# Performance work log

Measured on AMD Instinct MI355X. Metric: run time of the kernel, lower is better.

## Reference

```python
import jax, jax.numpy as jnp
import numpy as np

CODEBOOK_SIZE = 1024
EMBEDDING_DIM = 256
COMMITMENT_COST = 0.25


def setup_inputs() -> dict:
    key = jax.random.key(0)
    k1, k2 = jax.random.split(key)
    x = jax.random.normal(k1, (32, EMBEDDING_DIM, 32, 32), dtype=jnp.float32)
    # embedding initialized uniform(-1/K, 1/K) like the torch module
    embedding = jax.random.uniform(
        k2, (CODEBOOK_SIZE, EMBEDDING_DIM), dtype=jnp.float32,
        minval=-1.0 / CODEBOOK_SIZE, maxval=1.0 / CODEBOOK_SIZE)
    return {"x": x, "embedding": embedding}


def reference(x, embedding):
    # x: [B, C, H, W] -> inputs: [B, H, W, C]
    inputs = jnp.transpose(x, (0, 2, 3, 1))
    input_shape = inputs.shape
    flat = inputs.reshape(-1, EMBEDDING_DIM)  # [N, D]
    # squared L2 distances to codebook: [N, K]
    distances = (jnp.sum(flat ** 2, axis=1, keepdims=True)
                 + jnp.sum(embedding ** 2, axis=1)
                 - 2.0 * flat @ embedding.T)
    encoding_indices = jnp.argmin(distances, axis=1)  # [N]
    encodings = jax.nn.one_hot(encoding_indices, CODEBOOK_SIZE, dtype=jnp.float32)  # [N, K]
    # gather (same math as encodings @ embedding)
    quantized = embedding[encoding_indices].reshape(input_shape)  # [B, H, W, C]
    e_latent_loss = jnp.mean((jax.lax.stop_gradient(quantized) - inputs) ** 2)
    q_latent_loss = jnp.mean((quantized - jax.lax.stop_gradient(inputs)) ** 2)
    loss = q_latent_loss + COMMITMENT_COST * e_latent_loss
    # straight-through estimator
    quantized_st = inputs + jax.lax.stop_gradient(quantized - inputs)
    return (loss, jnp.transpose(quantized_st, (0, 3, 1, 2)), encodings)
```

## Files before the change

### kernel.cpp

```cpp
#include <hip/hip_runtime.h>
#include <cstdint>
#include <cstddef>

constexpr int B = 32, C = 256, H = 32, W = 32;
constexpr int NPTS = B * H * W;
constexpr int DIM  = 256;
constexpr int K    = 1024;
constexpr int QELEMS = B * C * H * W;
constexpr int CHW = C * H * W;

typedef __attribute__((ext_vector_type(8))) short s8v;
typedef __attribute__((ext_vector_type(4))) float f32x4;

#define GLD_LDS16(g, l)                                                        \
  __builtin_amdgcn_global_load_lds(                                            \
      (const __attribute__((address_space(1))) unsigned int*)(g),              \
      (__attribute__((address_space(3))) unsigned int*)(l), 16, 0, 0)

__device__ __forceinline__ unsigned short f2bf(float f) {
  unsigned u = __float_as_uint(f);
  return (unsigned short)((u + 0x7FFFu + ((u >> 16) & 1u)) >> 16);
}

__global__ __launch_bounds__(256) void prep_kernel(
    const float* __restrict__ x, const float* __restrict__ emb,
    unsigned short* __restrict__ ehi, float* __restrict__ esq,
    unsigned short* __restrict__ xhi, float* __restrict__ xsq,
    float* __restrict__ encz) {
  __shared__ float xls[DIM][32];
  const int t = threadIdx.x;
  const int bid = blockIdx.x;

  if (bid < 16) {
    float (*sums)[64] = (float (*)[64])xls;
    const int k = bid * 64 + (t & 63);
    const int seg = t >> 6;
    const float* er = emb + (size_t)k * DIM + seg * 64;
    float v[64];
    float4* v4 = (float4*)v;
#pragma unroll
    for (int i = 0; i < 16; ++i) v4[i] = *(const float4*)(er + i * 4);
    float s = 0.f;
#pragma unroll
    for (int i = 0; i < 64; ++i) s = fmaf(v[i], v[i], s);
    unsigned short* eo = ehi + (size_t)k * DIM + seg * 64;
#pragma unroll
    for (int i = 0; i < 8; ++i) {
      unsigned short h[8];
#pragma unroll
      for (int j = 0; j < 8; ++j) h[j] = f2bf(v[i * 8 + j]);
      *(s8v*)(eo + i * 8) = *(s8v*)h;
    }
    sums[seg][t & 63] = s;
    __syncthreads();
    if (t < 64)
      esq[bid * 64 + t] =
          ((sums[0][t] + sums[1][t]) + sums[2][t]) + sums[3][t];
    return;
  }

  const int u = bid - 16;
  const int g = u / 3, r = u - g * 3;

  if (r != 0) {
    const size_t bidx = (size_t)g * 2 + (r - 1);
    float* sl = encz + bidx * 16384;
    float4* b4 = (float4*)(sl + 3);
    const float4 z4 = {0.f, 0.f, 0.f, 0.f};
#pragma unroll
    for (int j = 0; j < 16; ++j) {
      const int idx = t + j * 256;
      if (idx < 4095) b4[idx] = z4;
    }
    if (t == 0) { sl[0] = 0.f; sl[1] = 0.f; sl[2] = 0.f; sl[16383] = 0.f; }
    return;
  }

  const int n0 = g * 32;
  const int bb = n0 >> 10, hw0 = n0 & 1023;
  const float* xb = x + (size_t)bb * CHW + hw0;
  const int lane = t & 63, w = t >> 6;
  const int row_off = lane >> 3;
  const int p4 = (lane & 7) * 4;
#pragma unroll
  for (int i = 0; i < 8; ++i) {
    const int c0 = w * 64 + i * 8;
    GLD_LDS16(xb + (size_t)(c0 + row_off) * 1024 + p4, &xls[c0][0]);
  }
  __syncthreads();

  if (t < 32) {
    float s = 0.f;
#pragma unroll 8
    for (int c = 0; c < 256; ++c) {
      const float v = xls[c][t];
      s = fmaf(v, v, s);
    }
    xsq[n0 + t] = s;
  }
  const int p2 = t & 31, cb = (t >> 5) * 32;
  unsigned short* xo = xhi + (size_t)(n0 + p2) * DIM + cb;
#pragma unroll
  for (int i = 0; i < 4; ++i) {
    unsigned short h[8];
#pragma unroll
    for (int j = 0; j < 8; ++j) h[j] = f2bf(xls[cb + i * 8 + j][p2]);
    *(s8v*)(xo + i * 8) = *(s8v*)h;
  }
}

constexpr float MARGIN = 1e-3f;
__global__ __launch_bounds__(256) void coarse_kernel(
    const unsigned short* __restrict__ xhi, const unsigned short* __restrict__ ehi,
    const float* __restrict__ esq, const float* __restrict__ xsq,
    float* __restrict__ part, unsigned int* __restrict__ cand) {
  __shared__ __align__(16) unsigned short xs[128][32];
  __shared__ __align__(16) unsigned short es[128][32];
  __shared__ float xsq_s[128], esq_s[128], thr_s[128];
  __shared__ unsigned long long red2[2][128];
  __shared__ unsigned int cntL[128];

  const int t = threadIdx.x;
  const int lane = t & 63, w = t >> 6;
  const int wn = (w & 1) * 64, wk = (w >> 1) * 64;
  const int col = lane & 15, quad = lane >> 4;
  const int nblk = blockIdx.x * 128;
  const int kblk = blockIdx.y * 128;

  if (t < 128) {
    xsq_s[t] = xsq[nblk + t];
    esq_s[t] = esq[kblk + t];
    cntL[t] = 0u;
  }

  f32x4 acc[4][4];
#pragma unroll
  for (int i = 0; i < 4; ++i)
#pragma unroll
    for (int j = 0; j < 4; ++j) acc[i][j] = (f32x4){0.f, 0.f, 0.f, 0.f};

  const int gl_row = lane >> 2;
  const int gl_c   = (lane & 3) * 8;

  for (int c0 = 0; c0 < DIM; c0 += 32) {
    __syncthreads();
#pragma unroll
    for (int i = 0; i < 2; ++i) {
      const int inst = w + 4 * i;
      const int row = inst * 16 + gl_row;
      GLD_LDS16(xhi + (size_t)(nblk + row) * DIM + c0 + gl_c, &xs[inst * 16][0]);
      GLD_LDS16(ehi + (size_t)(kblk + row) * DIM + c0 + gl_c, &es[inst * 16][0]);
    }
    __syncthreads();
    s8v a[4], b[4];
#pragma unroll
    for (int ti = 0; ti < 4; ++ti)
      a[ti] = *(const s8v*)&xs[wn + ti * 16 + col][quad * 8];
#pragma unroll
    for (int tj = 0; tj < 4; ++tj)
      b[tj] = *(const s8v*)&es[wk + tj * 16 + col][quad * 8];
#pragma unroll
    for (int ti = 0; ti < 4; ++ti)
#pragma unroll
      for (int tj = 0; tj < 4; ++tj)
        acc[ti][tj] = __builtin_amdgcn_mfma_f32_16x16x32_bf16(
            a[ti], b[tj], acc[ti][tj], 0, 0, 0);
  }

  unsigned long long nmin[4][4];
#pragma unroll
  for (int ti = 0; ti < 4; ++ti)
#pragma unroll
    for (int r = 0; r < 4; ++r) nmin[ti][r] = ~0ULL;
#pragma unroll
  for (int ti = 0; ti < 4; ++ti)
#pragma unroll
    for (int tj = 0; tj < 4; ++tj) {
      const int krel = wk + tj * 16 + col;
      const float eq = esq_s[krel];
#pragma unroll
      for (int r = 0; r < 4; ++r) {
        const int nl = wn + ti * 16 + quad * 4 + r;
        const float d = (xsq_s[nl] + eq) - 2.f * acc[ti][tj][r];
        const unsigned long long key =
            ((unsigned long long)__float_as_uint(d) << 32) |
            (unsigned)(kblk + krel);
        if (key < nmin[ti][r]) nmin[ti][r] = key;
      }
    }
#pragma unroll
  for (int o = 1; o < 16; o <<= 1)
#pragma unroll
    for (int ti = 0; ti < 4; ++ti)
#pragma unroll
      for (int r = 0; r < 4; ++r) {
        const unsigned long long v = __shfl_xor(nmin[ti][r], o, 64);
        if (v < nmin[ti][r]) nmin[ti][r] = v;
      }
  if (col == 0) {
#pragma unroll
    for (int ti = 0; ti < 4; ++ti)
#pragma unroll
      for (int r = 0; r < 4; ++r)
        red2[w >> 1][wn + ti * 16 + quad * 4 + r] = nmin[ti][r];
  }
  __syncthreads();
  if (t < 128) {
    const unsigned long long m0 = red2[0][t], m1 = red2[1][t];
    const unsigned long long m = (m1 < m0) ? m1 : m0;
    const float dmin = __uint_as_float((unsigned)(m >> 32));
    part[(size_t)(nblk + t) * 8 + blockIdx.y] = dmin;
    thr_s[t] = dmin + MARGIN;
  }
  __syncthreads();
#pragma unroll
  for (int ti = 0; ti < 4; ++ti)
#pragma unroll
    for (int tj = 0; tj < 4; ++tj) {
      const int krel = wk + tj * 16 + col;
      const float eq = esq_s[krel];
#pragma unroll
      for (int r = 0; r < 4; ++r) {
        const int nl = wn + ti * 16 + quad * 4 + r;
        const float d = (xsq_s[nl] + eq) - 2.f * acc[ti][tj][r];
        if (d <= thr_s[nl]) {
          const unsigned slot = atomicAdd(&cntL[nl], 1u);
          if (slot < 4u)
            cand[((size_t)(nblk + nl) * 8 + blockIdx.y) * 4 + slot] =
                (unsigned)(kblk + krel);
        }
      }
    }
  __syncthreads();
  if (t < 128) {
    unsigned c = cntL[t];
    const size_t base = ((size_t)(nblk + t) * 8 + blockIdx.y) * 4;
    if (c > 4u) { cand[base + 3] = 0xFFFFFFFEu; c = 3u; }
    for (unsigned s = c; s < 4u; ++s) cand[base + s] = 0xFFFFFFFFu;
  }
}

__global__ __launch_bounds__(256) void finish_kernel(
    const float* __restrict__ x, const float* __restrict__ emb,
    const float* __restrict__ esq, const float* __restrict__ xsq,
    const float* __restrict__ part, const unsigned int* __restrict__ cand,
    float* __restrict__ outq, float* __restrict__ enc,
    float* __restrict__ lws) {
  __shared__ __align__(16) float xls[DIM][17];
  __shared__ unsigned list[512];
  __shared__ unsigned long long best[16];
  __shared__ float thr_s[16];
  __shared__ float xsq_s[16];
  __shared__ float lred[4];
  __shared__ int ids[16];
  __shared__ int lcnt;

  const int t = threadIdx.x;
  const int n0 = blockIdx.x * 16;
  const int bb = n0 >> 10, hw0 = n0 & 1023;

  const float* xb = x + (size_t)bb * CHW + hw0;
  {
    const int p = t & 15, cs = t >> 4;
#pragma unroll 4
    for (int r = 0; r < 16; ++r) {
      const int c = r * 16 + cs;
      xls[c][p] = xb[(size_t)c * 1024 + p];
    }
  }
  if (t == 0) lcnt = 0;
  if (t < 16) {
    best[t] = ~0ULL;
    xsq_s[t] = xsq[n0 + t];
    const float4 p0 = *(const float4*)&part[(size_t)(n0 + t) * 8];
    const float4 p1 = *(const float4*)&part[(size_t)(n0 + t) * 8 + 4];
    float g = fminf(fminf(fminf(p0.x, p0.y), fminf(p0.z, p0.w)),
                    fminf(fminf(p1.x, p1.y), fminf(p1.z, p1.w)));
    thr_s[t] = g + MARGIN;
  }
  __syncthreads();

  if (t < 128) {
    const int nn = t >> 3, s = t & 7;
    const float pv = part[(size_t)(n0 + nn) * 8 + s];
    if (pv <= thr_s[nn]) {
      const uint4 c4 = *(const uint4*)&cand[((size_t)(n0 + nn) * 8 + s) * 4];
      const unsigned vs[4] = {c4.x, c4.y, c4.z, c4.w};
#pragma unroll
      for (int i = 0; i < 4; ++i) {
        const unsigned v = vs[i];
        if (v == 0xFFFFFFFFu) continue;
        const unsigned entry = (v == 0xFFFFFFFEu)
                                   ? ((unsigned)nn << 11) | 1024u | (unsigned)s
                                   : ((unsigned)nn << 11) | (v & 1023u);
        const int pos = atomicAdd(&lcnt, 1);
        if (pos < 512) list[pos] = entry;
      }
    }
  }
  __syncthreads();

  const int L = lcnt < 512 ? lcnt : 512;
  for (int e = t; e < L; e += 256) {
    const unsigned entry = list[e];
    const int p = entry >> 11;
    const float xq = xsq_s[p];
    int klo, khi;
    if (entry & 1024u) { const int s = entry & 7; klo = s * 128; khi = klo + 128; }
    else               { klo = entry & 1023u; khi = klo + 1; }
    for (int k = klo; k < khi; ++k) {
      const float* er = emb + (size_t)k * DIM;
      float dot = 0.f;
#pragma unroll 4
      for (int c4 = 0; c4 < DIM; c4 += 4) {
        const float4 e4 = *(const float4*)(er + c4);
        dot = fmaf(xls[c4 + 0][p], e4.x, dot);
        dot = fmaf(xls[c4 + 1][p], e4.y, dot);
        dot = fmaf(xls[c4 + 2][p], e4.z, dot);
        dot = fmaf(xls[c4 + 3][p], e4.w, dot);
      }
      const float t1 = xq + esq[k];
      const float d = t1 - 2.f * dot;
      const unsigned long long key =
          ((unsigned long long)__float_as_uint(d) << 32) | (unsigned)k;
      atomicMin(&best[p], key);
    }
  }
  __syncthreads();
  if (t < 16) ids[t] = (int)(best[t] & 0xFFFFFFFFu);
  __syncthreads();

  float lsum = 0.f;
  {
    const int p = t & 15, g = t >> 4;
    const int row = ids[p];
    const float* er = emb + (size_t)row * DIM + g * 16;
    float* ob = outq + (size_t)bb * CHW + hw0 + p;
#pragma unroll
    for (int i = 0; i < 4; ++i) {
      const float4 v = *(const float4*)(er + i * 4);
      const int c = g * 16 + i * 4;
      float d0 = v.x - xls[c + 0][p];
      float d1 = v.y - xls[c + 1][p];
      float d2 = v.z - xls[c + 2][p];
      float d3 = v.w - xls[c + 3][p];
      ob[(size_t)(c + 0) * 1024] = v.x;
      ob[(size_t)(c + 1) * 1024] = v.y;
      ob[(size_t)(c + 2) * 1024] = v.z;
      ob[(size_t)(c + 3) * 1024] = v.w;
      lsum = fmaf(d0, d0, lsum);
      lsum = fmaf(d1, d1, lsum);
      lsum = fmaf(d2, d2, lsum);
      lsum = fmaf(d3, d3, lsum);
    }
  }

  if (t < 16) enc[(size_t)(n0 + t) * K + ids[t]] = 1.0f;

  float s = lsum;
#pragma unroll
  for (int o = 32; o > 0; o >>= 1) s += __shfl_down(s, o, 64);
  if ((t & 63) == 0) lred[t >> 6] = s;
  __syncthreads();
  if (t == 0)
    lws[blockIdx.x] = ((lred[0] + lred[1]) + lred[2]) + lred[3];
}

__global__ __launch_bounds__(256) void loss_reduce(
    const float* __restrict__ lws, float* __restrict__ loss) {
  __shared__ float red[4];
  const int t = threadIdx.x;
  float s = 0.f;
#pragma unroll
  for (int i = 0; i < 8; ++i) s += lws[t + i * 256];
#pragma unroll
  for (int o = 32; o > 0; o >>= 1) s += __shfl_down(s, o, 64);
  if ((t & 63) == 0) red[t >> 6] = s;
  __syncthreads();
  if (t == 0)
    *loss = (((red[0] + red[1]) + red[2]) + red[3]) * (1.25f / (float)QELEMS);
}

extern "C" void kernel_launch(void* const* d_in, const int* in_sizes, int n_in,
                              void* d_out, int out_size, void* d_ws, size_t ws_size,
                              hipStream_t stream) {
  const float* x   = (const float*)d_in[0];
  const float* emb = (const float*)d_in[1];
  float* out  = (float*)d_out;
  float* loss = out;
  float* outq = out + 1;
  float* enc  = out + 1 + QELEMS;

  char* ws = (char*)d_ws;
  unsigned short* ehi  = (unsigned short*)ws;
  float*          esq  = (float*)(ws + 524288);
  float*          xsq  = (float*)(ws + 528384);
  float*          part = (float*)(ws + 659456);
  unsigned int*   cand = (unsigned int*)(ws + 1708032);
  unsigned short* xhi  = (unsigned short*)(ws + 5902336);
  float*          lws  = (float*)(ws + 22679552);

  prep_kernel<<<16 + 3072, 256, 0, stream>>>(x, emb, ehi, esq, xhi, xsq, enc);
  dim3 cg(NPTS / 128, 8);
  coarse_kernel<<<cg, 256, 0, stream>>>(xhi, ehi, esq, xsq, part, cand);
  finish_kernel<<<NPTS / 16, 256, 0, stream>>>(x, emb, esq, xsq, part, cand,
                                               outq, enc, lws);
  loss_reduce<<<1, 256, 0, stream>>>(lws, loss);
}
```

Measured before the change: 290.6 us.

## Split finish into resolve, one-hot write, and coalesced quantized-output kernels

```diff
diff --git a/kernel.cpp b/kernel.cpp
--- a/kernel.cpp
+++ b/kernel.cpp
@@ -25,8 +25,7 @@
 __global__ __launch_bounds__(256) void prep_kernel(
     const float* __restrict__ x, const float* __restrict__ emb,
     unsigned short* __restrict__ ehi, float* __restrict__ esq,
-    unsigned short* __restrict__ xhi, float* __restrict__ xsq,
-    float* __restrict__ encz) {
+    unsigned short* __restrict__ xhi, float* __restrict__ xsq) {
   __shared__ float xls[DIM][32];
   const int t = threadIdx.x;
   const int bid = blockIdx.x;
@@ -59,24 +58,7 @@
     return;
   }
 
-  const int u = bid - 16;
-  const int g = u / 3, r = u - g * 3;
-
-  if (r != 0) {
-    const size_t bidx = (size_t)g * 2 + (r - 1);
-    float* sl = encz + bidx * 16384;
-    float4* b4 = (float4*)(sl + 3);
-    const float4 z4 = {0.f, 0.f, 0.f, 0.f};
-#pragma unroll
-    for (int j = 0; j < 16; ++j) {
-      const int idx = t + j * 256;
-      if (idx < 4095) b4[idx] = z4;
-    }
-    if (t == 0) { sl[0] = 0.f; sl[1] = 0.f; sl[2] = 0.f; sl[16383] = 0.f; }
-    return;
-  }
-
-  const int n0 = g * 32;
+  const int n0 = (bid - 16) * 32;
   const int bb = n0 >> 10, hw0 = n0 & 1023;
   const float* xb = x + (size_t)bb * CHW + hw0;
   const int lane = t & 63, w = t >> 6;
@@ -240,19 +222,16 @@
   }
 }
 
-__global__ __launch_bounds__(256) void finish_kernel(
+__global__ __launch_bounds__(256) void resolve_kernel(
     const float* __restrict__ x, const float* __restrict__ emb,
     const float* __restrict__ esq, const float* __restrict__ xsq,
     const float* __restrict__ part, const unsigned int* __restrict__ cand,
-    float* __restrict__ outq, float* __restrict__ enc,
-    float* __restrict__ lws) {
+    int* __restrict__ ids_g) {
   __shared__ __align__(16) float xls[DIM][17];
   __shared__ unsigned list[512];
   __shared__ unsigned long long best[16];
   __shared__ float thr_s[16];
   __shared__ float xsq_s[16];
-  __shared__ float lred[4];
-  __shared__ int ids[16];
   __shared__ int lcnt;
 
   const int t = threadIdx.x;
@@ -327,35 +306,73 @@
     }
   }
   __syncthreads();
-  if (t < 16) ids[t] = (int)(best[t] & 0xFFFFFFFFu);
-  __syncthreads();
-
+  if (t < 16) ids_g[n0 + t] = (int)(best[t] & 0xFFFFFFFFu);
+}
+
+__global__ __launch_bounds__(256) void enc_kernel(
+    const int* __restrict__ ids_g, float* __restrict__ enc) {
+  __shared__ int ids_s[16];
+  const int t = threadIdx.x;
+  const int n0 = blockIdx.x * 16;
+  if (t < 16) ids_s[t] = ids_g[n0 + t];
+  __syncthreads();
+
+  float* sl = enc + (size_t)blockIdx.x * 16384;
+  float4* b4 = (float4*)(sl + 3);
+#pragma unroll
+  for (int j = 0; j < 16; ++j) {
+    const int idx = t + j * 256;
+    if (idx < 4095) {
+      const int lf = 3 + 4 * idx;
+      float4 v;
+      v.x = (((lf + 0) & 1023) == ids_s[(lf + 0) >> 10]) ? 1.f : 0.f;
+      v.y = (((lf + 1) & 1023) == ids_s[(lf + 1) >> 10]) ? 1.f : 0.f;
+      v.z = (((lf + 2) & 1023) == ids_s[(lf + 2) >> 10]) ? 1.f : 0.f;
+      v.w = (((lf + 3) & 1023) == ids_s[(lf + 3) >> 10]) ? 1.f : 0.f;
+      b4[idx] = v;
+    }
+  }
+  if (t == 0) {
+    sl[0] = (ids_s[0] == 0) ? 1.f : 0.f;
+    sl[1] = (ids_s[0] == 1) ? 1.f : 0.f;
+    sl[2] = (ids_s[0] == 2) ? 1.f : 0.f;
+    sl[16383] = (ids_s[15] == 1023) ? 1.f : 0.f;
+  }
+}
+
+__global__ __launch_bounds__(256) void outq_kernel(
+    const float* __restrict__ x, const float* __restrict__ emb,
+    const int* __restrict__ ids_g, float* __restrict__ outq,
+    float* __restrict__ lws) {
+  __shared__ int ids_s[1024];
+  __shared__ float lred[4];
+  const int t = threadIdx.x;
+  const int bb = blockIdx.x >> 5;
+  const int c0 = (blockIdx.x & 31) * 8;
+
+#pragma unroll
+  for (int i = 0; i < 4; ++i) ids_s[t + i * 256] = ids_g[bb * 1024 + t + i * 256];
+  __syncthreads();
+
+  const float* xb = x + (size_t)bb * CHW;
+  float* ob = outq + (size_t)bb * CHW;
   float lsum = 0.f;
-  {
-    const int p = t & 15, g = t >> 4;
-    const int row = ids[p];
-    const float* er = emb + (size_t)row * DIM + g * 16;
-    float* ob = outq + (size_t)bb * CHW + hw0 + p;
-#pragma unroll
-    for (int i = 0; i < 4; ++i) {
-      const float4 v = *(const float4*)(er + i * 4);
-      const int c = g * 16 + i * 4;
-      float d0 = v.x - xls[c + 0][p];
-      float d1 = v.y - xls[c + 1][p];
-      float d2 = v.z - xls[c + 2][p];
-      float d3 = v.w - xls[c + 3][p];
-      ob[(size_t)(c + 0) * 1024] = v.x;
-      ob[(size_t)(c + 1) * 1024] = v.y;
-      ob[(size_t)(c + 2) * 1024] = v.z;
-      ob[(size_t)(c + 3) * 1024] = v.w;
-      lsum = fmaf(d0, d0, lsum);
-      lsum = fmaf(d1, d1, lsum);
-      lsum = fmaf(d2, d2, lsum);
-      lsum = fmaf(d3, d3, lsum);
-    }
-  }
-
-  if (t < 16) enc[(size_t)(n0 + t) * K + ids[t]] = 1.0f;
+#pragma unroll
+  for (int i = 0; i < 4; ++i) {
+    const int hw = t + i * 256;
+    const int id = ids_s[hw];
+    const float* er = emb + (size_t)id * DIM + c0;
+    const float4 e0 = *(const float4*)(er);
+    const float4 e1 = *(const float4*)(er + 4);
+    const float q[8] = {e0.x, e0.y, e0.z, e0.w, e1.x, e1.y, e1.z, e1.w};
+#pragma unroll
+    for (int ci = 0; ci < 8; ++ci) {
+      const float xv = xb[(size_t)(c0 + ci) * 1024 + hw];
+      ob[(size_t)(c0 + ci) * 1024 + hw] = q[ci];
+      const float d = q[ci] - xv;
+      lsum = fmaf(d, d, lsum);
+    }
+  }
 
   float s = lsum;
 #pragma unroll
@@ -372,7 +389,7 @@
   const int t = threadIdx.x;
   float s = 0.f;
 #pragma unroll
-  for (int i = 0; i < 8; ++i) s += lws[t + i * 256];
+  for (int i = 0; i < 4; ++i) s += lws[t + i * 256];
 #pragma unroll
   for (int o = 32; o > 0; o >>= 1) s += __shfl_down(s, o, 64);
   if ((t & 63) == 0) red[t >> 6] = s;
@@ -399,11 +416,14 @@
   unsigned int*   cand = (unsigned int*)(ws + 1708032);
   unsigned short* xhi  = (unsigned short*)(ws + 5902336);
   float*          lws  = (float*)(ws + 22679552);
-
-  prep_kernel<<<16 + 3072, 256, 0, stream>>>(x, emb, ehi, esq, xhi, xsq, enc);
+  int*            ids  = (int*)(ws + 22683648);
+
+  prep_kernel<<<16 + 1024, 256, 0, stream>>>(x, emb, ehi, esq, xhi, xsq);
   dim3 cg(NPTS / 128, 8);
   coarse_kernel<<<cg, 256, 0, stream>>>(xhi, ehi, esq, xsq, part, cand);
-  finish_kernel<<<NPTS / 16, 256, 0, stream>>>(x, emb, esq, xsq, part, cand,
-                                               outq, enc, lws);
+  resolve_kernel<<<NPTS / 16, 256, 0, stream>>>(x, emb, esq, xsq, part, cand,
+                                                ids);
+  enc_kernel<<<NPTS / 16, 256, 0, stream>>>(ids, enc);
+  outq_kernel<<<1024, 256, 0, stream>>>(x, emb, ids, outq, lws);
   loss_reduce<<<1, 256, 0, stream>>>(lws, loss);
 }
```

Result: no change. 293.2 us (+0.9%).
